# Performance work log

Hardware: AMD Instinct MI355X
Metric: run time of the kernel (lower is better)

Reference implementation:

```python
import jax, jax.numpy as jnp
import numpy as np


def _gcn_conv(x, W, b, src, dst, n):
    """PyG-style GCNConv: x' = D^{-1/2} A_hat D^{-1/2} (x W) + b, with self-loops."""
    xw = x @ W                                   # [N, out]
    deg = jax.ops.segment_sum(jnp.ones_like(dst, dtype=x.dtype), dst, num_segments=n)
    dinv = jnp.where(deg > 0, jax.lax.rsqrt(deg), 0.0)
    norm = dinv[src] * dinv[dst]                 # [E+N]
    msgs = norm[:, None] * xw[src]               # gather + normalize
    out = jax.ops.segment_sum(msgs, dst, num_segments=n)  # scatter-add
    return out + b


def setup_inputs() -> dict:
    key = jax.random.key(0)
    k1, k2, k3, k4 = jax.random.split(key, 4)
    N, E, D, H, C = 500000, 8000000, 100, 16, 20
    x = jax.random.normal(k1, (N, D), dtype=jnp.float32)
    edge_index = jax.random.randint(k2, (2, E), 0, N, dtype=jnp.int64)
    W1 = jax.random.normal(k3, (D, H), dtype=jnp.float32) * (1.0 / np.sqrt(D))
    b1 = jnp.zeros((H,), dtype=jnp.float32)
    W2 = jax.random.normal(k4, (H, C), dtype=jnp.float32) * (1.0 / np.sqrt(H))
    b2 = jnp.zeros((C,), dtype=jnp.float32)
    return {"x": x, "edge_index": edge_index, "W1": W1, "b1": b1, "W2": W2, "b2": b2}


def reference(x, edge_index, W1, b1, W2, b2):
    n = x.shape[0]
    loops = jnp.arange(n, dtype=edge_index.dtype)
    src = jnp.concatenate([edge_index[0], loops])  # add self-loops
    dst = jnp.concatenate([edge_index[1], loops])
    h = _gcn_conv(x, W1, b1, src, dst, n)
    h = jax.nn.relu(h)
    # dropout is identity in eval mode (F.dropout with training=False)
    h = _gcn_conv(h, W2, b2, src, dst, n)
    return jax.nn.log_softmax(h, axis=1)
```

## Files before the change

### kernel.cpp

```cpp
#include <hip/hip_runtime.h>
#include <hip/hip_bf16.h>
#include <hip/hip_fp16.h>

#define NDIM 100
#define HDIM 16
#define CDIM 20

#define BSH2   10
#define BMASK2 ((1 << BSH2) - 1)
#define NB2MAX 768
#define CH2    16384
#define LBUF_CAP 18432

__device__ inline float2 h2f2(unsigned u) {
    __half2 h = *reinterpret_cast<__half2*>(&u);
    return __half22float2(h);
}
__device__ inline unsigned f2h2(float a, float b) {
    __half2 h = __floats2half2_rn(a, b);
    return *reinterpret_cast<unsigned*>(&h);
}


__global__ __launch_bounds__(256) void histA(const int* __restrict__ dst,
                                             int* __restrict__ bcnt,
                                             int E, int NB2) {
    __shared__ int lh[NB2MAX];
    for (int t = threadIdx.x; t < NB2MAX; t += 256) lh[t] = 0;
    __syncthreads();

    int base = blockIdx.x * 8192;
    int endv = min(base + 8192, E);
    for (int e = base + threadIdx.x; e < endv; e += 256)
        atomicAdd(&lh[dst[e] >> BSH2], 1);
    __syncthreads();

    for (int t = threadIdx.x; t < NB2; t += 256) {
        int v = lh[t];
        if (v) atomicAdd(&bcnt[t], v);
    }
}


__global__ __launch_bounds__(256) void scan_k2(int* __restrict__ bsum,
                                               int* __restrict__ gcur, int nb) {
    __shared__ int part[256];
    int t = threadIdx.x;
    int base = t * 8;
    int loc[8];
    int s = 0;
#pragma unroll
    for (int k = 0; k < 8; ++k) {
        int idx = base + k;
        loc[k] = (idx < nb) ? bsum[idx] : 0;
        s += loc[k];
    }
    part[t] = s;
    __syncthreads();
    for (int off = 1; off < 256; off <<= 1) {
        int add = (t >= off) ? part[t - off] : 0;
        __syncthreads();
        part[t] += add;
        __syncthreads();
    }
    int run = (t > 0) ? part[t - 1] : 0;
#pragma unroll
    for (int k = 0; k < 8; ++k) {
        int idx = base + k;
        if (idx < nb) { bsum[idx] = run; gcur[idx] = run; }
        run += loc[k];
    }
}


__global__ __launch_bounds__(1024) void scatter_sort(const int* __restrict__ src,
                                                     const int* __restrict__ dst,
                                                     int* __restrict__ gcur,
                                                     unsigned* __restrict__ tmp,
                                                     int E, int NB2) {
    __shared__ unsigned lbuf[CH2];
    __shared__ int lcnt[1024];
    __shared__ int lst[1024];
    __shared__ int gb[1024];
    const int t = threadIdx.x;

    lcnt[t] = 0;
    __syncthreads();

    int base = blockIdx.x * CH2;
    int endv = min(base + CH2, E);
    for (int e = base + t; e < endv; e += 1024)
        atomicAdd(&lcnt[dst[e] >> BSH2], 1);
    __syncthreads();

    int c = lcnt[t];
    lst[t] = c;
    __syncthreads();
    for (int off = 1; off < 1024; off <<= 1) {
        int add = (t >= off) ? lst[t - off] : 0;
        __syncthreads();
        lst[t] += add;
        __syncthreads();
    }
    int ex = lst[t] - c;

    int gbase = 0;
    if (t < NB2 && c > 0) gbase = atomicAdd(&gcur[t], c);
    gb[t]   = gbase;
    lst[t]  = ex;
    lcnt[t] = ex;
    __syncthreads();

    for (int e = base + t; e < endv; e += 1024) {
        int d = dst[e];
        int b = d >> BSH2;
        int pos = atomicAdd(&lcnt[b], 1);
        lbuf[pos] = ((unsigned)src[e] << BSH2) | (unsigned)(d & BMASK2);
    }
    __syncthreads();

    int grp = t >> 4, lane = t & 15;
    for (int b = grp; b < NB2; b += 64) {
        int s0 = lst[b], g0 = gb[b];
        int len = lcnt[b] - s0;
        for (int k = lane; k < len; k += 16)
            tmp[(size_t)g0 + k] = lbuf[s0 + k];
    }
}


__global__ __launch_bounds__(1024) void binC(const unsigned* __restrict__ tmp,
                                             const int* __restrict__ B0,
                                             int2* __restrict__ seg,
                                             float* __restrict__ dinv,
                                             int* __restrict__ esrc,
                                             int N, int E, int NB2) {
    __shared__ int lbuf[LBUF_CAP];
    __shared__ int lh[1024];
    __shared__ int lcur[1024];
    int b = blockIdx.x, t = threadIdx.x;

    lh[t] = 0;
    __syncthreads();

    int lo = B0[b];
    int hi = (b + 1 < NB2) ? B0[b + 1] : E;

    for (int i = lo + t; i < hi; i += 1024)
        atomicAdd(&lh[tmp[i] & BMASK2], 1);
    __syncthreads();

    int cnt = lh[t];
    __syncthreads();
    for (int off = 1; off < 1024; off <<= 1) {
        int add = (t >= off) ? lh[t - off] : 0;
        __syncthreads();
        lh[t] += add;
        __syncthreads();
    }
    int end   = lo + lh[t];
    int start = end - cnt;

    int node = (b << BSH2) + t;
    if (node < N) {
        seg[node]  = make_int2(end, cnt);
        dinv[node] = rsqrtf((float)(cnt + 1));
    }
    lcur[t] = start - lo;
    __syncthreads();

    bool fits = (hi - lo) <= LBUF_CAP;
    if (fits) {
        for (int i = lo + t; i < hi; i += 1024) {
            unsigned v = tmp[i];
            int pos = atomicAdd(&lcur[v & BMASK2], 1);
            lbuf[pos] = (int)(v >> BSH2);
        }
        __syncthreads();
        for (int i = lo + t; i < hi; i += 1024)
            esrc[i] = lbuf[i - lo];
    } else {
        for (int i = lo + t; i < hi; i += 1024) {
            unsigned v = tmp[i];
            int pos = atomicAdd(&lcur[v & BMASK2], 1);
            esrc[(size_t)lo + pos] = (int)(v >> BSH2);
        }
    }
}


__global__ __launch_bounds__(256) void xw1_kernel(const float* __restrict__ x,
                                                  const float* __restrict__ W1,
                                                  const float* __restrict__ dinv,
                                                  __half* __restrict__ xw1h, int N) {
    __shared__ float Ws[NDIM * HDIM];
    for (int t = threadIdx.x; t < NDIM * HDIM; t += 256) Ws[t] = W1[t];
    __syncthreads();

    const int ln = threadIdx.x >> 2;
    const int q  = threadIdx.x & 3;
    const int node = blockIdx.x * 64 + ln;
    if (node >= N) return;

    const float4* xr  = reinterpret_cast<const float4*>(x + (size_t)node * NDIM);
    const float4* Ws4 = reinterpret_cast<const float4*>(Ws);

    float4 acc = make_float4(0.f, 0.f, 0.f, 0.f);
#pragma unroll
    for (int kk = 0; kk < NDIM / 4; ++kk) {
        float4 xv = xr[kk];
        float xs[4] = {xv.x, xv.y, xv.z, xv.w};
#pragma unroll
        for (int c = 0; c < 4; ++c) {
            float4 w = Ws4[(kk * 4 + c) * 4 + q];
            acc.x += xs[c] * w.x;
            acc.y += xs[c] * w.y;
            acc.z += xs[c] * w.z;
            acc.w += xs[c] * w.w;
        }
    }
    float dn = dinv[node];
    uint2 o;
    o.x = f2h2(dn * acc.x, dn * acc.y);
    o.y = f2h2(dn * acc.z, dn * acc.w);
    reinterpret_cast<uint2*>(xw1h)[(size_t)node * 4 + q] = o;
}


__global__ __launch_bounds__(256) void gather1(const int* __restrict__ esrc,
                                               const int2* __restrict__ seg,
                                               const float* __restrict__ dinv,
                                               const __half* __restrict__ xw1h,
                                               const float* __restrict__ b1,
                                               __half* __restrict__ hsh, int N) {
    int g  = threadIdx.x >> 2;
    int f4 = threadIdx.x & 3;
    int n  = blockIdx.x * 64 + g;
    if (n >= N) return;

    int2 cd   = seg[n];
    int end   = cd.x;
    int start = end - cd.y;
    float dn  = dinv[n];

    const uint2* T = reinterpret_cast<const uint2*>(xw1h);
    uint2 sv = T[(size_t)n * 4 + f4];
    float2 s01 = h2f2(sv.x), s23 = h2f2(sv.y);
    float4 a0 = make_float4(s01.x, s01.y, s23.x, s23.y);
    float4 a1 = make_float4(0.f, 0.f, 0.f, 0.f);

    int j = start;
    for (; j + 3 < end; j += 4) {
        int i0 = esrc[j + 0], i1 = esrc[j + 1];
        int i2 = esrc[j + 2], i3 = esrc[j + 3];
        uint2 v0 = T[(size_t)i0 * 4 + f4];
        uint2 v1 = T[(size_t)i1 * 4 + f4];
        uint2 v2 = T[(size_t)i2 * 4 + f4];
        uint2 v3 = T[(size_t)i3 * 4 + f4];
        float2 p, q;
        p = h2f2(v0.x); q = h2f2(v0.y);
        a0.x += p.x; a0.y += p.y; a0.z += q.x; a0.w += q.y;
        p = h2f2(v1.x); q = h2f2(v1.y);
        a1.x += p.x; a1.y += p.y; a1.z += q.x; a1.w += q.y;
        p = h2f2(v2.x); q = h2f2(v2.y);
        a0.x += p.x; a0.y += p.y; a0.z += q.x; a0.w += q.y;
        p = h2f2(v3.x); q = h2f2(v3.y);
        a1.x += p.x; a1.y += p.y; a1.z += q.x; a1.w += q.y;
    }
    for (; j < end; ++j) {
        int s = esrc[j];
        uint2 v = T[(size_t)s * 4 + f4];
        float2 p = h2f2(v.x), q = h2f2(v.y);
        a0.x += p.x; a0.y += p.y; a0.z += q.x; a0.w += q.y;
    }
    float4 acc = make_float4(a0.x + a1.x, a0.y + a1.y, a0.z + a1.z, a0.w + a1.w);
    float4 bv = reinterpret_cast<const float4*>(b1)[f4];
    float hx = dn * fmaxf(dn * acc.x + bv.x, 0.f);
    float hy = dn * fmaxf(dn * acc.y + bv.y, 0.f);
    float hz = dn * fmaxf(dn * acc.z + bv.z, 0.f);
    float hw = dn * fmaxf(dn * acc.w + bv.w, 0.f);
    uint2 o;
    o.x = f2h2(hx, hy);
    o.y = f2h2(hz, hw);
    reinterpret_cast<uint2*>(hsh)[(size_t)n * 4 + f4] = o;
}


__global__ __launch_bounds__(256) void gather2(const int* __restrict__ esrc,
                                               const int2* __restrict__ seg,
                                               const float* __restrict__ dinv,
                                               const __half* __restrict__ hsh,
                                               float* __restrict__ agg2, int N) {
    int g  = threadIdx.x >> 2;
    int f4 = threadIdx.x & 3;
    int n  = blockIdx.x * 64 + g;
    if (n >= N) return;

    int2 cd   = seg[n];
    int end   = cd.x;
    int start = end - cd.y;
    float dn  = dinv[n];

    const uint2* T = reinterpret_cast<const uint2*>(hsh);
    uint2 sv = T[(size_t)n * 4 + f4];
    float2 s01 = h2f2(sv.x), s23 = h2f2(sv.y);
    float4 a0 = make_float4(s01.x, s01.y, s23.x, s23.y);
    float4 a1 = make_float4(0.f, 0.f, 0.f, 0.f);

    int j = start;
    for (; j + 3 < end; j += 4) {
        int i0 = esrc[j + 0], i1 = esrc[j + 1];
        int i2 = esrc[j + 2], i3 = esrc[j + 3];
        uint2 v0 = T[(size_t)i0 * 4 + f4];
        uint2 v1 = T[(size_t)i1 * 4 + f4];
        uint2 v2 = T[(size_t)i2 * 4 + f4];
        uint2 v3 = T[(size_t)i3 * 4 + f4];
        float2 p, q;
        p = h2f2(v0.x); q = h2f2(v0.y);
        a0.x += p.x; a0.y += p.y; a0.z += q.x; a0.w += q.y;
        p = h2f2(v1.x); q = h2f2(v1.y);
        a1.x += p.x; a1.y += p.y; a1.z += q.x; a1.w += q.y;
        p = h2f2(v2.x); q = h2f2(v2.y);
        a0.x += p.x; a0.y += p.y; a0.z += q.x; a0.w += q.y;
        p = h2f2(v3.x); q = h2f2(v3.y);
        a1.x += p.x; a1.y += p.y; a1.z += q.x; a1.w += q.y;
    }
    for (; j < end; ++j) {
        int s = esrc[j];
        uint2 v = T[(size_t)s * 4 + f4];
        float2 p = h2f2(v.x), q = h2f2(v.y);
        a0.x += p.x; a0.y += p.y; a0.z += q.x; a0.w += q.y;
    }
    float4 o;
    o.x = dn * (a0.x + a1.x);
    o.y = dn * (a0.y + a1.y);
    o.z = dn * (a0.z + a1.z);
    o.w = dn * (a0.w + a1.w);
    reinterpret_cast<float4*>(agg2)[(size_t)n * 4 + f4] = o;
}


__global__ __launch_bounds__(256) void final_kernel(const float* __restrict__ agg2,
                                                    const float* __restrict__ W2,
                                                    const float* __restrict__ b2,
                                                    float* __restrict__ out, int N) {
    __shared__ float W2t[CDIM * HDIM];
    __shared__ float b2s[CDIM];
    for (int t = threadIdx.x; t < CDIM * HDIM; t += 256) {
        int j = t / HDIM, k = t % HDIM;
        W2t[t] = W2[k * CDIM + j];
    }
    for (int t = threadIdx.x; t < CDIM; t += 256) b2s[t] = b2[t];
    __syncthreads();

    int n = blockIdx.x * 256 + threadIdx.x;
    if (n >= N) return;

    float a[HDIM];
    const float4* a4 = reinterpret_cast<const float4*>(agg2 + (size_t)n * HDIM);
#pragma unroll
    for (int c = 0; c < HDIM / 4; ++c) {
        float4 v = a4[c];
        a[4 * c + 0] = v.x; a[4 * c + 1] = v.y;
        a[4 * c + 2] = v.z; a[4 * c + 3] = v.w;
    }
    float o[CDIM];
#pragma unroll
    for (int j = 0; j < CDIM; ++j) {
        const float4* w4 = reinterpret_cast<const float4*>(W2t + j * HDIM);
        float s = b2s[j];
#pragma unroll
        for (int c = 0; c < HDIM / 4; ++c) {
            float4 w = w4[c];
            s += a[4 * c + 0] * w.x + a[4 * c + 1] * w.y +
                 a[4 * c + 2] * w.z + a[4 * c + 3] * w.w;
        }
        o[j] = s;
    }
    float m = o[0];
#pragma unroll
    for (int j = 1; j < CDIM; ++j) m = fmaxf(m, o[j]);
    float s = 0.f;
#pragma unroll
    for (int j = 0; j < CDIM; ++j) s += __expf(o[j] - m);
    float l = __logf(s);
    float4* out4 = reinterpret_cast<float4*>(out + (size_t)n * CDIM);
#pragma unroll
    for (int c = 0; c < CDIM / 4; ++c)
        out4[c] = make_float4(o[4 * c + 0] - m - l, o[4 * c + 1] - m - l,
                              o[4 * c + 2] - m - l, o[4 * c + 3] - m - l);
}


extern "C" void kernel_launch(void* const* d_in, const int* in_sizes, int n_in,
                              void* d_out, int out_size, void* d_ws, size_t ws_size,
                              hipStream_t stream) {
    const float* x  = (const float*)d_in[0];
    const int* edge = (const int*)d_in[1];
    const float* W1 = (const float*)d_in[2];
    const float* b1 = (const float*)d_in[3];
    const float* W2 = (const float*)d_in[4];
    const float* b2 = (const float*)d_in[5];
    float* out = (float*)d_out;

    const int N = in_sizes[0] / NDIM;
    const int E = in_sizes[1] / 2;
    const int* src = edge;
    const int* dst = edge + E;

    const int tb = 256;
    const int nbN = (N + tb - 1) / tb;
    const int NB2 = (N + BMASK2) >> BSH2;

    char* ws = (char*)d_ws;
    size_t off = 0;
    int2*     seg    = (int2*)(ws + off);   off += (size_t)N * 8;
    float*    dinv   = (float*)(ws + off);  off += (size_t)N * 4;
    __half*   xw1h   = (__half*)(ws + off); off += (size_t)N * HDIM * 2;
    __half*   hsh    = (__half*)(ws + off); off += (size_t)N * HDIM * 2;
    float*    agg2   = (float*)(ws + off);  off += (size_t)N * HDIM * 4;
    int*      esrc   = (int*)(ws + off);    off += (size_t)E * 4;
    int*      bcnt   = (int*)(ws + off);    off += (size_t)NB2MAX * 4;
    int*      gcur   = (int*)(ws + off);    off += (size_t)NB2MAX * 4;

    unsigned* tmp = (unsigned*)agg2;

    hipMemsetAsync(bcnt, 0, (size_t)NB2 * 4, stream);
    histA<<<(E + 8191) / 8192, tb, 0, stream>>>(dst, bcnt, E, NB2);
    scan_k2<<<1, tb, 0, stream>>>(bcnt, gcur, NB2);
    scatter_sort<<<(E + CH2 - 1) / CH2, 1024, 0, stream>>>(src, dst, gcur, tmp, E, NB2);
    binC<<<NB2, 1024, 0, stream>>>(tmp, bcnt, seg, dinv, esrc, N, E, NB2);

    xw1_kernel<<<(N + 63) / 64, tb, 0, stream>>>(x, W1, dinv, xw1h, N);

    gather1<<<(N + 63) / 64, tb, 0, stream>>>(esrc, seg, dinv, xw1h, b1, hsh, N);

    gather2<<<(N + 63) / 64, tb, 0, stream>>>(esrc, seg, dinv, hsh, agg2, N);

    final_kernel<<<nbN, tb, 0, stream>>>(agg2, W2, b2, out, N);
}
```

Measured before the change: 700.6 us.

## Split each node's edges into source-range chunks with block barriers for gather locality

binC now buckets every node's incoming edges into four ranges of source id (by the high bits), storing per-chunk counts packed in a widened int4 segment record. It also drops the shared-memory staging buffer and scatters directly to global esrc. The gather kernels walk the chunks in order and place a __syncthreads between them, so all threads in a block read from the same slice of the feature table at roughly the same time, improving cache hit rates on random gathers. The cost is extra barriers that stall on the slowest node, a larger segment record, and more scattered global writes in binC.

```diff
diff --git a/kernel.cpp b/kernel.cpp
--- a/kernel.cpp
+++ b/kernel.cpp
@@ -10,7 +10,7 @@
 #define BMASK2 ((1 << BSH2) - 1)
 #define NB2MAX 768
 #define CH2    16384
-#define LBUF_CAP 18432
+#define CHSH   17
 
 __device__ inline float2 h2f2(unsigned u) {
     __half2 h = *reinterpret_cast<__half2*>(&u);
@@ -131,60 +131,58 @@
 
 __global__ __launch_bounds__(1024) void binC(const unsigned* __restrict__ tmp,
                                              const int* __restrict__ B0,
-                                             int2* __restrict__ seg,
+                                             int4* __restrict__ segc,
                                              float* __restrict__ dinv,
                                              int* __restrict__ esrc,
                                              int N, int E, int NB2) {
-    __shared__ int lbuf[LBUF_CAP];
-    __shared__ int lh[1024];
-    __shared__ int lcur[1024];
+    __shared__ int lh[4096];
+    __shared__ int part[1024];
     int b = blockIdx.x, t = threadIdx.x;
 
-    lh[t] = 0;
+    for (int i = t; i < 4096; i += 1024) lh[i] = 0;
     __syncthreads();
 
     int lo = B0[b];
     int hi = (b + 1 < NB2) ? B0[b + 1] : E;
 
-    for (int i = lo + t; i < hi; i += 1024)
-        atomicAdd(&lh[tmp[i] & BMASK2], 1);
-    __syncthreads();
-
-    int cnt = lh[t];
+    for (int i = lo + t; i < hi; i += 1024) {
+        unsigned v = tmp[i];
+        unsigned ch = min(v >> (BSH2 + CHSH), 3u);
+        atomicAdd(&lh[((v & BMASK2) << 2) | ch], 1);
+    }
+    __syncthreads();
+
+    int c0 = lh[4 * t], c1 = lh[4 * t + 1], c2 = lh[4 * t + 2], c3 = lh[4 * t + 3];
+    int cnt = c0 + c1 + c2 + c3;
+    part[t] = cnt;
     __syncthreads();
     for (int off = 1; off < 1024; off <<= 1) {
-        int add = (t >= off) ? lh[t - off] : 0;
-        __syncthreads();
-        lh[t] += add;
-        __syncthreads();
-    }
-    int end   = lo + lh[t];
-    int start = end - cnt;
+        int add = (t >= off) ? part[t - off] : 0;
+        __syncthreads();
+        part[t] += add;
+        __syncthreads();
+    }
+    int endl = part[t];
+    int st   = endl - cnt;
+
+    lh[4 * t]     = lo + st;
+    lh[4 * t + 1] = lo + st + c0;
+    lh[4 * t + 2] = lo + st + c0 + c1;
+    lh[4 * t + 3] = lo + st + c0 + c1 + c2;
 
     int node = (b << BSH2) + t;
     if (node < N) {
-        seg[node]  = make_int2(end, cnt);
+        segc[node] = make_int4(lo + endl, cnt, (c0 << 16) | c1, (c2 << 16) | c3);
         dinv[node] = rsqrtf((float)(cnt + 1));
     }
-    lcur[t] = start - lo;
-    __syncthreads();
-
-    bool fits = (hi - lo) <= LBUF_CAP;
-    if (fits) {
-        for (int i = lo + t; i < hi; i += 1024) {
-            unsigned v = tmp[i];
-            int pos = atomicAdd(&lcur[v & BMASK2], 1);
-            lbuf[pos] = (int)(v >> BSH2);
-        }
-        __syncthreads();
-        for (int i = lo + t; i < hi; i += 1024)
-            esrc[i] = lbuf[i - lo];
-    } else {
-        for (int i = lo + t; i < hi; i += 1024) {
-            unsigned v = tmp[i];
-            int pos = atomicAdd(&lcur[v & BMASK2], 1);
-            esrc[(size_t)lo + pos] = (int)(v >> BSH2);
-        }
+    __syncthreads();
+
+    for (int i = lo + t; i < hi; i += 1024) {
+        unsigned v = tmp[i];
+        unsigned srcv = v >> BSH2;
+        unsigned ch = min(srcv >> CHSH, 3u);
+        int pos = atomicAdd(&lh[((v & BMASK2) << 2) | ch], 1);
+        esrc[pos] = (int)srcv;
     }
 }
 
@@ -228,7 +226,7 @@
 
 
 __global__ __launch_bounds__(256) void gather1(const int* __restrict__ esrc,
-                                               const int2* __restrict__ seg,
+                                               const int4* __restrict__ segc,
                                                const float* __restrict__ dinv,
                                                const __half* __restrict__ xw1h,
                                                const float* __restrict__ b1,
@@ -236,107 +234,125 @@
     int g  = threadIdx.x >> 2;
     int f4 = threadIdx.x & 3;
     int n  = blockIdx.x * 64 + g;
-    if (n >= N) return;
-
-    int2 cd   = seg[n];
-    int end   = cd.x;
-    int start = end - cd.y;
-    float dn  = dinv[n];
+    bool active = (n < N);
 
     const uint2* T = reinterpret_cast<const uint2*>(xw1h);
-    uint2 sv = T[(size_t)n * 4 + f4];
-    float2 s01 = h2f2(sv.x), s23 = h2f2(sv.y);
-    float4 a0 = make_float4(s01.x, s01.y, s23.x, s23.y);
+    int4 sc = make_int4(0, 0, 0, 0);
+    float dn = 0.f;
+    float4 a0 = make_float4(0.f, 0.f, 0.f, 0.f);
     float4 a1 = make_float4(0.f, 0.f, 0.f, 0.f);
-
-    int j = start;
-    for (; j + 3 < end; j += 4) {
-        int i0 = esrc[j + 0], i1 = esrc[j + 1];
-        int i2 = esrc[j + 2], i3 = esrc[j + 3];
-        uint2 v0 = T[(size_t)i0 * 4 + f4];
-        uint2 v1 = T[(size_t)i1 * 4 + f4];
-        uint2 v2 = T[(size_t)i2 * 4 + f4];
-        uint2 v3 = T[(size_t)i3 * 4 + f4];
-        float2 p, q;
-        p = h2f2(v0.x); q = h2f2(v0.y);
-        a0.x += p.x; a0.y += p.y; a0.z += q.x; a0.w += q.y;
-        p = h2f2(v1.x); q = h2f2(v1.y);
-        a1.x += p.x; a1.y += p.y; a1.z += q.x; a1.w += q.y;
-        p = h2f2(v2.x); q = h2f2(v2.y);
-        a0.x += p.x; a0.y += p.y; a0.z += q.x; a0.w += q.y;
-        p = h2f2(v3.x); q = h2f2(v3.y);
-        a1.x += p.x; a1.y += p.y; a1.z += q.x; a1.w += q.y;
-    }
-    for (; j < end; ++j) {
-        int s = esrc[j];
-        uint2 v = T[(size_t)s * 4 + f4];
-        float2 p = h2f2(v.x), q = h2f2(v.y);
-        a0.x += p.x; a0.y += p.y; a0.z += q.x; a0.w += q.y;
-    }
-    float4 acc = make_float4(a0.x + a1.x, a0.y + a1.y, a0.z + a1.z, a0.w + a1.w);
-    float4 bv = reinterpret_cast<const float4*>(b1)[f4];
-    float hx = dn * fmaxf(dn * acc.x + bv.x, 0.f);
-    float hy = dn * fmaxf(dn * acc.y + bv.y, 0.f);
-    float hz = dn * fmaxf(dn * acc.z + bv.z, 0.f);
-    float hw = dn * fmaxf(dn * acc.w + bv.w, 0.f);
-    uint2 o;
-    o.x = f2h2(hx, hy);
-    o.y = f2h2(hz, hw);
-    reinterpret_cast<uint2*>(hsh)[(size_t)n * 4 + f4] = o;
+    if (active) {
+        sc = segc[n];
+        dn = dinv[n];
+        uint2 sv = T[(size_t)n * 4 + f4];
+        float2 s01 = h2f2(sv.x), s23 = h2f2(sv.y);
+        a0 = make_float4(s01.x, s01.y, s23.x, s23.y);
+    }
+    int lens[4] = {sc.z >> 16, sc.z & 0xffff, sc.w >> 16, sc.w & 0xffff};
+    int j = sc.x - sc.y;
+
+    for (int c = 0; c < 4; ++c) {
+        int e2 = j + lens[c];
+        for (; j + 3 < e2; j += 4) {
+            int i0 = esrc[j + 0], i1 = esrc[j + 1];
+            int i2 = esrc[j + 2], i3 = esrc[j + 3];
+            uint2 v0 = T[(size_t)i0 * 4 + f4];
+            uint2 v1 = T[(size_t)i1 * 4 + f4];
+            uint2 v2 = T[(size_t)i2 * 4 + f4];
+            uint2 v3 = T[(size_t)i3 * 4 + f4];
+            float2 p, q;
+            p = h2f2(v0.x); q = h2f2(v0.y);
+            a0.x += p.x; a0.y += p.y; a0.z += q.x; a0.w += q.y;
+            p = h2f2(v1.x); q = h2f2(v1.y);
+            a1.x += p.x; a1.y += p.y; a1.z += q.x; a1.w += q.y;
+            p = h2f2(v2.x); q = h2f2(v2.y);
+            a0.x += p.x; a0.y += p.y; a0.z += q.x; a0.w += q.y;
+            p = h2f2(v3.x); q = h2f2(v3.y);
+            a1.x += p.x; a1.y += p.y; a1.z += q.x; a1.w += q.y;
+        }
+        for (; j < e2; ++j) {
+            int s = esrc[j];
+            uint2 v = T[(size_t)s * 4 + f4];
+            float2 p = h2f2(v.x), q = h2f2(v.y);
+            a0.x += p.x; a0.y += p.y; a0.z += q.x; a0.w += q.y;
+        }
+        if (c < 3) __syncthreads();
+    }
+    if (active) {
+        float4 acc = make_float4(a0.x + a1.x, a0.y + a1.y, a0.z + a1.z, a0.w + a1.w);
+        float4 bv = reinterpret_cast<const float4*>(b1)[f4];
+        float hx = dn * fmaxf(dn * acc.x + bv.x, 0.f);
+        float hy = dn * fmaxf(dn * acc.y + bv.y, 0.f);
+        float hz = dn * fmaxf(dn * acc.z + bv.z, 0.f);
+        float hw = dn * fmaxf(dn * acc.w + bv.w, 0.f);
+        uint2 o;
+        o.x = f2h2(hx, hy);
+        o.y = f2h2(hz, hw);
+        reinterpret_cast<uint2*>(hsh)[(size_t)n * 4 + f4] = o;
+    }
 }
 
 
 __global__ __launch_bounds__(256) void gather2(const int* __restrict__ esrc,
-                                               const int2* __restrict__ seg,
+                                               const int4* __restrict__ segc,
                                                const float* __restrict__ dinv,
                                                const __half* __restrict__ hsh,
                                                float* __restrict__ agg2, int N) {
     int g  = threadIdx.x >> 2;
     int f4 = threadIdx.x & 3;
     int n  = blockIdx.x * 64 + g;
-    if (n >= N) return;
-
-    int2 cd   = seg[n];
-    int end   = cd.x;
-    int start = end - cd.y;
-    float dn  = dinv[n];
+    bool active = (n < N);
 
     const uint2* T = reinterpret_cast<const uint2*>(hsh);
-    uint2 sv = T[(size_t)n * 4 + f4];
-    float2 s01 = h2f2(sv.x), s23 = h2f2(sv.y);
-    float4 a0 = make_float4(s01.x, s01.y, s23.x, s23.y);
+    int4 sc = make_int4(0, 0, 0, 0);
+    float dn = 0.f;
+    float4 a0 = make_float4(0.f, 0.f, 0.f, 0.f);
     float4 a1 = make_float4(0.f, 0.f, 0.f, 0.f);
-
-    int j = start;
-    for (; j + 3 < end; j += 4) {
-        int i0 = esrc[j + 0], i1 = esrc[j + 1];
-        int i2 = esrc[j + 2], i3 = esrc[j + 3];
-        uint2 v0 = T[(size_t)i0 * 4 + f4];
-        uint2 v1 = T[(size_t)i1 * 4 + f4];
-        uint2 v2 = T[(size_t)i2 * 4 + f4];
-        uint2 v3 = T[(size_t)i3 * 4 + f4];
-        float2 p, q;
-        p = h2f2(v0.x); q = h2f2(v0.y);
-        a0.x += p.x; a0.y += p.y; a0.z += q.x; a0.w += q.y;
-        p = h2f2(v1.x); q = h2f2(v1.y);
-        a1.x += p.x; a1.y += p.y; a1.z += q.x; a1.w += q.y;
-        p = h2f2(v2.x); q = h2f2(v2.y);
-        a0.x += p.x; a0.y += p.y; a0.z += q.x; a0.w += q.y;
-        p = h2f2(v3.x); q = h2f2(v3.y);
-        a1.x += p.x; a1.y += p.y; a1.z += q.x; a1.w += q.y;
-    }
-    for (; j < end; ++j) {
-        int s = esrc[j];
-        uint2 v = T[(size_t)s * 4 + f4];
-        float2 p = h2f2(v.x), q = h2f2(v.y);
-        a0.x += p.x; a0.y += p.y; a0.z += q.x; a0.w += q.y;
-    }
-    float4 o;
-    o.x = dn * (a0.x + a1.x);
-    o.y = dn * (a0.y + a1.y);
-    o.z = dn * (a0.z + a1.z);
-    o.w = dn * (a0.w + a1.w);
-    reinterpret_cast<float4*>(agg2)[(size_t)n * 4 + f4] = o;
+    if (active) {
+        sc = segc[n];
+        dn = dinv[n];
+        uint2 sv = T[(size_t)n * 4 + f4];
+        float2 s01 = h2f2(sv.x), s23 = h2f2(sv.y);
+        a0 = make_float4(s01.x, s01.y, s23.x, s23.y);
+    }
+    int lens[4] = {sc.z >> 16, sc.z & 0xffff, sc.w >> 16, sc.w & 0xffff};
+    int j = sc.x - sc.y;
+
+    for (int c = 0; c < 4; ++c) {
+        int e2 = j + lens[c];
+        for (; j + 3 < e2; j += 4) {
+            int i0 = esrc[j + 0], i1 = esrc[j + 1];
+            int i2 = esrc[j + 2], i3 = esrc[j + 3];
+            uint2 v0 = T[(size_t)i0 * 4 + f4];
+            uint2 v1 = T[(size_t)i1 * 4 + f4];
+            uint2 v2 = T[(size_t)i2 * 4 + f4];
+            uint2 v3 = T[(size_t)i3 * 4 + f4];
+            float2 p, q;
+            p = h2f2(v0.x); q = h2f2(v0.y);
+            a0.x += p.x; a0.y += p.y; a0.z += q.x; a0.w += q.y;
+            p = h2f2(v1.x); q = h2f2(v1.y);
+            a1.x += p.x; a1.y += p.y; a1.z += q.x; a1.w += q.y;
+            p = h2f2(v2.x); q = h2f2(v2.y);
+            a0.x += p.x; a0.y += p.y; a0.z += q.x; a0.w += q.y;
+            p = h2f2(v3.x); q = h2f2(v3.y);
+            a1.x += p.x; a1.y += p.y; a1.z += q.x; a1.w += q.y;
+        }
+        for (; j < e2; ++j) {
+            int s = esrc[j];
+            uint2 v = T[(size_t)s * 4 + f4];
+            float2 p = h2f2(v.x), q = h2f2(v.y);
+            a0.x += p.x; a0.y += p.y; a0.z += q.x; a0.w += q.y;
+        }
+        if (c < 3) __syncthreads();
+    }
+    if (active) {
+        float4 o;
+        o.x = dn * (a0.x + a1.x);
+        o.y = dn * (a0.y + a1.y);
+        o.z = dn * (a0.z + a1.z);
+        o.w = dn * (a0.w + a1.w);
+        reinterpret_cast<float4*>(agg2)[(size_t)n * 4 + f4] = o;
+    }
 }
 
 
@@ -414,7 +430,7 @@
 
     char* ws = (char*)d_ws;
     size_t off = 0;
-    int2*     seg    = (int2*)(ws + off);   off += (size_t)N * 8;
+    int4*     segc   = (int4*)(ws + off);   off += (size_t)N * 16;
     float*    dinv   = (float*)(ws + off);  off += (size_t)N * 4;
     __half*   xw1h   = (__half*)(ws + off); off += (size_t)N * HDIM * 2;
     __half*   hsh    = (__half*)(ws + off); off += (size_t)N * HDIM * 2;
@@ -429,13 +445,13 @@
     histA<<<(E + 8191) / 8192, tb, 0, stream>>>(dst, bcnt, E, NB2);
     scan_k2<<<1, tb, 0, stream>>>(bcnt, gcur, NB2);
     scatter_sort<<<(E + CH2 - 1) / CH2, 1024, 0, stream>>>(src, dst, gcur, tmp, E, NB2);
-    binC<<<NB2, 1024, 0, stream>>>(tmp, bcnt, seg, dinv, esrc, N, E, NB2);
+    binC<<<NB2, 1024, 0, stream>>>(tmp, bcnt, segc, dinv, esrc, N, E, NB2);
 
     xw1_kernel<<<(N + 63) / 64, tb, 0, stream>>>(x, W1, dinv, xw1h, N);
 
-    gather1<<<(N + 63) / 64, tb, 0, stream>>>(esrc, seg, dinv, xw1h, b1, hsh, N);
-
-    gather2<<<(N + 63) / 64, tb, 0, stream>>>(esrc, seg, dinv, hsh, agg2, N);
+    gather1<<<(N + 63) / 64, tb, 0, stream>>>(esrc, segc, dinv, xw1h, b1, hsh, N);
+
+    gather2<<<(N + 63) / 64, tb, 0, stream>>>(esrc, segc, dinv, hsh, agg2, N);
 
     final_kernel<<<nbN, tb, 0, stream>>>(agg2, W2, b2, out, N);
 }
```

Result: no change. 707.4 us (+1.0%).
